# Optimization experiments

Hardware: AMD Instinct MI355X
Metric: run time of the kernel (lower is better)

Reference implementation:

```python
import jax, jax.numpy as jnp
import numpy as np

ALPHA = 0.2          # LeakyReLU negative slope
NEG = -9e15          # masking value from the torch source


def _gat_multihead(x, adj, W, a):
    """All nheads GATLayers (concat=True math, elu applied by caller).
    x: [B,N,F], adj: [B,N,N], W: [H,F,O], a: [H,2O]. Returns [B,H,N,O].
    Note a_input @ a decomposes as h_i.a[:O] + h_j.a[O:], so we never
    materialize the O(N^2 * 2O) pairwise concat tensor."""
    h = jnp.einsum('bnf,hfo->bhno', x, W)            # [B,H,N,O]
    O = h.shape[-1]
    s1 = jnp.einsum('bhno,ho->bhn', h, a[:, :O])     # h_i . a_src
    s2 = jnp.einsum('bhno,ho->bhn', h, a[:, O:])     # h_j . a_dst
    e = jax.nn.leaky_relu(s1[..., :, None] + s2[..., None, :], ALPHA)  # [B,H,N,N]
    att = jax.nn.softmax(jnp.where(adj[:, None] > 0, e, NEG), axis=-1)
    return jnp.einsum('bhij,bhjo->bhio', att, h)


def _gat_single(x, adj, W, a):
    """out_att GATLayer (concat=False, no elu). W: [F,O], a: [2O]."""
    h = jnp.einsum('bnf,fo->bno', x, W)
    O = W.shape[-1]
    s1 = h @ a[:O]
    s2 = h @ a[O:]
    e = jax.nn.leaky_relu(s1[:, :, None] + s2[:, None, :], ALPHA)
    att = jax.nn.softmax(jnp.where(adj > 0, e, NEG), axis=-1)
    return jnp.einsum('bij,bjo->bio', att, h)


def setup_inputs() -> dict:
    key = jax.random.key(0)
    ks = jax.random.split(key, 10)
    B, N, F = 2, 2048, 768
    H, O = 8, 256
    x = jax.random.normal(ks[0], (B, N, F), dtype=jnp.float32)
    # sparse-ish binary adjacency (adj>0 is all that matters) + self loops
    adj = (jax.random.uniform(ks[1], (B, N, N)) < 0.05).astype(jnp.float32)
    adj = jnp.maximum(adj, jnp.eye(N, dtype=jnp.float32)[None])
    mask = jnp.ones((B, N, 1), dtype=jnp.float32)  # unused by GAT.forward
    s = 0.05
    W_heads = jax.random.normal(ks[2], (H, F, O), dtype=jnp.float32) * s
    a_heads = jax.random.normal(ks[3], (H, 2 * O), dtype=jnp.float32) * s
    W_out = jax.random.normal(ks[4], (H * O, O), dtype=jnp.float32) * s
    a_out = jax.random.normal(ks[5], (2 * O,), dtype=jnp.float32) * s
    W_lin = jax.random.normal(ks[6], (O, H * O), dtype=jnp.float32) * s  # nn.Linear weight [out,in]
    b_lin = jnp.zeros((O,), dtype=jnp.float32)
    W_ln = jax.random.normal(ks[7], (O, O), dtype=jnp.float32) * s
    b_ln = jnp.zeros((O,), dtype=jnp.float32)
    return {"x": x, "adj": adj, "mask": mask, "W_heads": W_heads,
            "a_heads": a_heads, "W_out": W_out, "a_out": a_out,
            "W_lin": W_lin, "b_lin": b_lin, "W_ln": W_ln, "b_ln": b_ln}


def reference(x, adj, mask, W_heads, a_heads, W_out, a_out, W_lin, b_lin, W_ln, b_ln):
    # layer 0: multi-head GAT, elu, concat over heads (dropout=0 in eval)
    hp = jax.nn.elu(_gat_multihead(x, adj, W_heads, a_heads))  # [B,H,N,O]
    B, H, N, O = hp.shape
    x1 = jnp.transpose(hp, (0, 2, 1, 3)).reshape(B, N, H * O)
    # layer 1: residual linear + out_att (concat=False)
    x2 = x1 @ W_lin.T + b_lin + _gat_single(x1, adj, W_out, a_out)
    # final: relu(ln(x))
    return jax.nn.relu(x2 @ W_ln.T + b_ln)
```

## Files before the change

kernel.cpp:

```cpp
#include <hip/hip_runtime.h>
#include <hip/hip_bf16.h>

constexpr int Bb = 2, Nn = 2048, Ff = 768, Hh = 8, Oo = 256;

typedef __attribute__((ext_vector_type(8)))  short   short8;
typedef __attribute__((ext_vector_type(16))) float   f32x16;
typedef __attribute__((ext_vector_type(4)))  unsigned short ushort4_t;

__device__ inline unsigned short f2bf(float f) {
    unsigned u = __float_as_uint(f);
    u = (u + 0x7FFFu + ((u >> 16) & 1u)) >> 16;
    return (unsigned short)u;
}

__device__ inline void wfrag_kn_body(
        const float* __restrict__ W, unsigned short* __restrict__ out,
        int K, int N, int fblk, int t) {
    int f = fblk * 4 + (t >> 6);
    int slot = t & 63, kh = slot >> 5, lm = slot & 31;
    int nfk = K >> 4;
    int nt = f / nfk, kt = f - nt * nfk;
    const float* wp = W + (size_t)(kt * 16 + kh * 8) * N + nt * 32 + lm;
    ushort4_t o0, o1;
    o0.x = f2bf(wp[0]);             o0.y = f2bf(wp[(size_t)N]);
    o0.z = f2bf(wp[2 * (size_t)N]); o0.w = f2bf(wp[3 * (size_t)N]);
    o1.x = f2bf(wp[4 * (size_t)N]); o1.y = f2bf(wp[5 * (size_t)N]);
    o1.z = f2bf(wp[6 * (size_t)N]); o1.w = f2bf(wp[7 * (size_t)N]);
    unsigned short* op = out + (size_t)f * 512 + slot * 8;
    *(ushort4_t*)op = o0;
    *(ushort4_t*)(op + 4) = o1;
}

__device__ inline void wfrag_nk_body(
        const float* __restrict__ W, unsigned short* __restrict__ out,
        int K, int fblk, int t) {
    int f = fblk * 4 + (t >> 6);
    int slot = t & 63, kh = slot >> 5, lm = slot & 31;
    int nfk = K >> 4;
    int nt = f / nfk, kt = f - nt * nfk;
    const float* wp = W + (size_t)(nt * 32 + lm) * K + kt * 16 + kh * 8;
    float4 a = *(const float4*)wp, b = *(const float4*)(wp + 4);
    ushort4_t o0, o1;
    o0.x = f2bf(a.x); o0.y = f2bf(a.y); o0.z = f2bf(a.z); o0.w = f2bf(a.w);
    o1.x = f2bf(b.x); o1.y = f2bf(b.y); o1.z = f2bf(b.z); o1.w = f2bf(b.w);
    unsigned short* op = out + (size_t)f * 512 + slot * 8;
    *(ushort4_t*)op = o0;
    *(ushort4_t*)(op + 4) = o1;
}

__global__ __launch_bounds__(256) void prep_misc_kernel(
        const float* __restrict__ adj, unsigned long long* __restrict__ bits,
        const float* __restrict__ x, unsigned short* __restrict__ x_bf,
        const float* __restrict__ W_heads, unsigned short* __restrict__ WhF,
        const float* __restrict__ W_out,   unsigned short* __restrict__ WoF,
        const float* __restrict__ W_lin,   unsigned short* __restrict__ WlF,
        const float* __restrict__ W_ln,    unsigned short* __restrict__ WnF) {
    int blk = blockIdx.x, t = threadIdx.x;
    if (blk < 32768) {
        size_t gid = (size_t)blk * 256 + t;
        float v = adj[gid];
        unsigned long long m = __ballot(v > 0.f);
        if ((t & 63) == 0) bits[gid >> 6] = m;
    } else if (blk < 35840) {
        size_t i = (size_t)(blk - 32768) * 256 + t;
        float4 v = ((const float4*)x)[i];
        ushort4_t o;
        o.x = f2bf(v.x); o.y = f2bf(v.y); o.z = f2bf(v.z); o.w = f2bf(v.w);
        ((ushort4_t*)x_bf)[i] = o;
    } else if (blk < 36608) {
        int idx = blk - 35840;
        int head = idx / 96, fblk = idx - head * 96;
        wfrag_kn_body(W_heads + (size_t)head * Ff * Oo, WhF + (size_t)head * 384 * 512,
                      Ff, Oo, fblk, t);
    } else if (blk < 36864) {
        wfrag_kn_body(W_out, WoF, Hh * Oo, Oo, blk - 36608, t);
    } else if (blk < 37120) {
        wfrag_nk_body(W_lin, WlF, Hh * Oo, blk - 36864, t);
    } else {
        wfrag_nk_body(W_ln, WnF, Oo, blk - 37120, t);
    }
}

template<int SWAPZ>
__global__ __launch_bounds__(256) void gemm32_kernel(
        const unsigned short* __restrict__ A, int K, long long sA, int bAshift,
        const unsigned short* __restrict__ BF, long long sB, int bmask,
        float* __restrict__ C, long long sC,
        unsigned short* __restrict__ CF, long long sCF, int Mtot,
        const float* __restrict__ bias, int mode,
        const float* __restrict__ aall, int amask,
        float* __restrict__ E1p, float* __restrict__ E1n, float2* __restrict__ E2pn) {
    int z  = SWAPZ ? blockIdx.x : blockIdx.z;
    int mx = SWAPZ ? blockIdx.y : blockIdx.x;
    A  += (size_t)(z >> bAshift) * sA;
    BF += (size_t)(z & bmask) * sB;
    if (C) C += (size_t)z * sC;
    if (CF) CF += (size_t)z * sCF;
    int m0 = mx * 32;
    int t = threadIdx.x;
    int wv = t >> 6, lane = t & 63;
    int lm = lane & 31, kh = lane >> 5;
    int nfk = K >> 4;
    __shared__ __align__(16) unsigned short As[32][136];
    f32x16 acc[2] = {};
    int sr = t >> 3, sc2 = (t & 7) * 16;
    const unsigned short* ag  = A + (size_t)(m0 + sr) * K + sc2;
    const unsigned short* bg0 = BF + (size_t)(wv * 2) * nfk * 512;
    const unsigned short* bg1 = bg0 + (size_t)nfk * 512;
    for (int k0 = 0; k0 < K; k0 += 128) {
        *(short8*)&As[sr][sc2]     = *(const short8*)(ag + k0);
        *(short8*)&As[sr][sc2 + 8] = *(const short8*)(ag + k0 + 8);
        int kt0 = k0 >> 4;
        __syncthreads();
#pragma unroll
        for (int s = 0; s < 8; ++s) {
            short8 a0 = *(const short8*)&As[lm][s * 16 + kh * 8];
            short8 b0 = *(const short8*)(bg0 + (size_t)(kt0 + s) * 512 + lane * 8);
            short8 b1 = *(const short8*)(bg1 + (size_t)(kt0 + s) * 512 + lane * 8);
            acc[0] = __builtin_amdgcn_mfma_f32_32x32x16_bf16(a0, b0, acc[0], 0, 0, 0);
            acc[1] = __builtin_amdgcn_mfma_f32_32x32x16_bf16(a0, b1, acc[1], 0, 0, 0);
        }
        __syncthreads();
    }
#pragma unroll
    for (int nt = 0; nt < 2; ++nt) {
        int colg = wv * 64 + nt * 32 + lm;
        float bv = (mode == 2) ? bias[colg] : 0.f;
        if (C) {
#pragma unroll
            for (int reg = 0; reg < 16; ++reg) {
                int rl = 4 * kh + (reg & 3) + 8 * (reg >> 2);
                float v = acc[nt][reg];
                if (mode == 2) { v += bv; v = fmaxf(v, 0.f); }
                C[(size_t)(m0 + rl) * 256 + colg] = v;
            }
        }
        if (mode == 1) {
#pragma unroll
            for (int q = 0; q < 4; ++q) {
                int kt = m0 / 16 + (q >> 1);
                size_t fi = ((size_t)(colg >> 5) * (Mtot / 16) + kt) * 512 +
                            ((q & 1) * 32 + (colg & 31)) * 8 + kh * 4;
                ushort4_t pk;
                pk.x = f2bf(acc[nt][q * 4 + 0]);
                pk.y = f2bf(acc[nt][q * 4 + 1]);
                pk.z = f2bf(acc[nt][q * 4 + 2]);
                pk.w = f2bf(acc[nt][q * 4 + 3]);
                *(ushort4_t*)(CF + fi) = pk;
            }
        }
    }
    if (aall) {
        const float* av = aall + (size_t)(z & amask) * 512;
        float a1v0 = av[wv * 64 + lm],       a1v1 = av[wv * 64 + 32 + lm];
        float a2v0 = av[256 + wv * 64 + lm], a2v1 = av[256 + wv * 64 + 32 + lm];
        float* sbuf = (float*)As;
#pragma unroll
        for (int reg = 0; reg < 16; ++reg) {
            int rl = 4 * kh + (reg & 3) + 8 * (reg >> 2);
            float v1 = acc[0][reg] * a1v0 + acc[1][reg] * a1v1;
            float v2 = acc[0][reg] * a2v0 + acc[1][reg] * a2v1;
#pragma unroll
            for (int m = 1; m <= 16; m <<= 1) {
                v1 += __shfl_xor(v1, m, 64);
                v2 += __shfl_xor(v2, m, 64);
            }
            if (lm == 0) { sbuf[rl * 8 + wv] = v1; sbuf[rl * 8 + 4 + wv] = v2; }
        }
        __syncthreads();
        if (t < 32) {
            float s1 = sbuf[t * 8] + sbuf[t * 8 + 1] + sbuf[t * 8 + 2] + sbuf[t * 8 + 3];
            float s2 = sbuf[t * 8 + 4] + sbuf[t * 8 + 5] + sbuf[t * 8 + 6] + sbuf[t * 8 + 7];
            size_t ei = (size_t)z * Nn + m0 + t;
            E1p[ei] = __expf(s1);
            E1n[ei] = __expf(0.2f * s1);
            E2pn[ei] = make_float2(__expf(s2), __expf(0.2f * s2));
        }
    }
}

__global__ __launch_bounds__(256) void gemm32_dual_kernel(
        const unsigned short* __restrict__ A, int K, long long sA,
        const unsigned short* __restrict__ BF,
        unsigned short* __restrict__ h2f, float* __restrict__ lin,
        const float* __restrict__ a_out,
        float* __restrict__ E1p, float* __restrict__ E1n, float2* __restrict__ E2pn) {
    int b = blockIdx.z, ng = blockIdx.y;
    A += (size_t)b * sA;
    int nfk = K >> 4;
    BF += (size_t)ng * 8 * nfk * 512;
    int m0 = blockIdx.x * 32;
    int t = threadIdx.x;
    int wv = t >> 6, lane = t & 63;
    int lm = lane & 31, kh = lane >> 5;
    __shared__ __align__(16) unsigned short As[32][136];
    f32x16 acc[2] = {};
    int sr = t >> 3, sc2 = (t & 7) * 16;
    const unsigned short* ag  = A + (size_t)(m0 + sr) * K + sc2;
    const unsigned short* bg0 = BF + (size_t)(wv * 2) * nfk * 512;
    const unsigned short* bg1 = bg0 + (size_t)nfk * 512;
    for (int k0 = 0; k0 < K; k0 += 128) {
        *(short8*)&As[sr][sc2]     = *(const short8*)(ag + k0);
        *(short8*)&As[sr][sc2 + 8] = *(const short8*)(ag + k0 + 8);
        int kt0 = k0 >> 4;
        __syncthreads();
#pragma unroll
        for (int s = 0; s < 8; ++s) {
            short8 a0 = *(const short8*)&As[lm][s * 16 + kh * 8];
            short8 b0 = *(const short8*)(bg0 + (size_t)(kt0 + s) * 512 + lane * 8);
            short8 b1 = *(const short8*)(bg1 + (size_t)(kt0 + s) * 512 + lane * 8);
            acc[0] = __builtin_amdgcn_mfma_f32_32x32x16_bf16(a0, b0, acc[0], 0, 0, 0);
            acc[1] = __builtin_amdgcn_mfma_f32_32x32x16_bf16(a0, b1, acc[1], 0, 0, 0);
        }
        __syncthreads();
    }
    if (ng == 1) {
        float* C = lin + (size_t)b * Nn * 256;
#pragma unroll
        for (int nt = 0; nt < 2; ++nt) {
            int colg = wv * 64 + nt * 32 + lm;
#pragma unroll
            for (int reg = 0; reg < 16; ++reg) {
                int rl = 4 * kh + (reg & 3) + 8 * (reg >> 2);
                C[(size_t)(m0 + rl) * 256 + colg] = acc[nt][reg];
            }
        }
    } else {
        unsigned short* CF = h2f + (size_t)b * 524288;
#pragma unroll
        for (int nt = 0; nt < 2; ++nt) {
            int colg = wv * 64 + nt * 32 + lm;
#pragma unroll
            for (int q = 0; q < 4; ++q) {
                int kt = m0 / 16 + (q >> 1);
                size_t fi = ((size_t)(colg >> 5) * 128 + kt) * 512 +
                            ((q & 1) * 32 + (colg & 31)) * 8 + kh * 4;
                ushort4_t pk;
                pk.x = f2bf(acc[nt][q * 4 + 0]);
                pk.y = f2bf(acc[nt][q * 4 + 1]);
                pk.z = f2bf(acc[nt][q * 4 + 2]);
                pk.w = f2bf(acc[nt][q * 4 + 3]);
                *(ushort4_t*)(CF + fi) = pk;
            }
        }
        float a1v0 = a_out[wv * 64 + lm],       a1v1 = a_out[wv * 64 + 32 + lm];
        float a2v0 = a_out[256 + wv * 64 + lm], a2v1 = a_out[256 + wv * 64 + 32 + lm];
        float* sbuf = (float*)As;
#pragma unroll
        for (int reg = 0; reg < 16; ++reg) {
            int rl = 4 * kh + (reg & 3) + 8 * (reg >> 2);
            float v1 = acc[0][reg] * a1v0 + acc[1][reg] * a1v1;
            float v2 = acc[0][reg] * a2v0 + acc[1][reg] * a2v1;
#pragma unroll
            for (int m = 1; m <= 16; m <<= 1) {
                v1 += __shfl_xor(v1, m, 64);
                v2 += __shfl_xor(v2, m, 64);
            }
            if (lm == 0) { sbuf[rl * 8 + wv] = v1; sbuf[rl * 8 + 4 + wv] = v2; }
        }
        __syncthreads();
        if (t < 32) {
            float s1 = sbuf[t * 8] + sbuf[t * 8 + 1] + sbuf[t * 8 + 2] + sbuf[t * 8 + 3];
            float s2 = sbuf[t * 8 + 4] + sbuf[t * 8 + 5] + sbuf[t * 8 + 6] + sbuf[t * 8 + 7];
            size_t ei = (size_t)b * Nn + m0 + t;
            E1p[ei] = __expf(s1);
            E1n[ei] = __expf(0.2f * s1);
            E2pn[ei] = make_float2(__expf(s2), __expf(0.2f * s2));
        }
    }
}

__global__ __launch_bounds__(256) void gemm32_final_kernel(
        const float* __restrict__ pacc, const float* __restrict__ plsum,
        const float* __restrict__ lin, const float* __restrict__ b_lin,
        const unsigned short* __restrict__ BF, const float* __restrict__ b_ln,
        float* __restrict__ out) {
    int b = blockIdx.z;
    int m0 = blockIdx.x * 32;
    int t = threadIdx.x;
    int wv = t >> 6, lane = t & 63;
    int lm = lane & 31, kh = lane >> 5;
    constexpr int nfk = 16;
    __shared__ __align__(16) unsigned short As[32][136];
    f32x16 acc[2] = {};
    int sr = t >> 3, sc2 = (t & 7) * 16;
    int row = m0 + sr;
    int BN = Bb * Nn;
    size_t prow = (size_t)b * Nn + row;
    float li = 1.f / (plsum[prow] + plsum[prow + BN] + plsum[prow + 2 * BN] + plsum[prow + 3 * BN]);
    size_t ps4 = (size_t)Bb * Nn * 256;
    const unsigned short* bg0 = BF + (size_t)(wv * 2) * nfk * 512;
    const unsigned short* bg1 = bg0 + (size_t)nfk * 512;
    for (int k0 = 0; k0 < 256; k0 += 128) {
        int o = k0 + sc2;
        size_t pidx = prow * 256 + o;
#pragma unroll
        for (int g = 0; g < 4; ++g) {
            float4 s4 = *(const float4*)(pacc + pidx + 4 * g);
#pragma unroll
            for (int k = 1; k < 4; ++k) {
                float4 q = *(const float4*)(pacc + k * ps4 + pidx + 4 * g);
                s4.x += q.x; s4.y += q.y; s4.z += q.z; s4.w += q.w;
            }
            float4 lv = *(const float4*)(lin + pidx + 4 * g);
            float4 bv = *(const float4*)(b_lin + o + 4 * g);
            ushort4_t pk;
            pk.x = f2bf(s4.x * li + lv.x + bv.x);
            pk.y = f2bf(s4.y * li + lv.y + bv.y);
            pk.z = f2bf(s4.z * li + lv.z + bv.z);
            pk.w = f2bf(s4.w * li + lv.w + bv.w);
            *(ushort4_t*)&As[sr][sc2 + 4 * g] = pk;
        }
        int kt0 = k0 >> 4;
        __syncthreads();
#pragma unroll
        for (int s = 0; s < 8; ++s) {
            short8 a0 = *(const short8*)&As[lm][s * 16 + kh * 8];
            short8 b0 = *(const short8*)(bg0 + (size_t)(kt0 + s) * 512 + lane * 8);
            short8 b1 = *(const short8*)(bg1 + (size_t)(kt0 + s) * 512 + lane * 8);
            acc[0] = __builtin_amdgcn_mfma_f32_32x32x16_bf16(a0, b0, acc[0], 0, 0, 0);
            acc[1] = __builtin_amdgcn_mfma_f32_32x32x16_bf16(a0, b1, acc[1], 0, 0, 0);
        }
        __syncthreads();
    }
    float* C = out + (size_t)b * Nn * 256;
#pragma unroll
    for (int nt = 0; nt < 2; ++nt) {
        int colg = wv * 64 + nt * 32 + lm;
        float bv = b_ln[colg];
#pragma unroll
        for (int reg = 0; reg < 16; ++reg) {
            int rl = 4 * kh + (reg & 3) + 8 * (reg >> 2);
            float v = fmaxf(acc[nt][reg] + bv, 0.f);
            C[(size_t)(m0 + rl) * 256 + colg] = v;
        }
    }
}

template<int JLEN, int MODE, int SWAPXY>
__global__ __launch_bounds__(256, 4) void attn_v8_kernel(
        const unsigned short* __restrict__ hfrag,
        const unsigned* __restrict__ bits,
        const float* __restrict__ E1p, const float* __restrict__ E1n,
        const float2* __restrict__ E2pn,
        unsigned short* __restrict__ outbf, int ldo,
        float* __restrict__ pacc, float* __restrict__ plsum,
        int hshift) {
    constexpr int W = JLEN / 32, NC = JLEN / 64, ABS = W + 1;
    int it = SWAPXY ? blockIdx.y : blockIdx.x;
    int bh = SWAPXY ? blockIdx.x : blockIdx.y;
    int js = blockIdx.z;
    int b = bh >> hshift, hd = bh & ((1 << hshift) - 1);
    int i0 = it * 32, jbase = js * JLEN;
    int kt0 = js * (JLEN / 16);
    int t = threadIdx.x, lane = t & 63;
    int wv = t >> 6, lm = lane & 31, kh = lane >> 5;
    int ti = t & 31, jq = t >> 5;

    __shared__ unsigned ab[32 * ABS];
    __shared__ __align__(16) unsigned short ps[2][32][64];
    __shared__ float lred[32][9];
    __shared__ float linv[32];

    const unsigned* bb = bits + ((size_t)b * Nn + i0) * 64 + (jbase >> 5);
    for (int k = t; k < 32 * W; k += 256) {
        int r = k / W, w0 = k - r * W;
        ab[r * ABS + w0] = bb[(size_t)r * 64 + w0];
    }
    __syncthreads();

    float e1p = E1p[(size_t)bh * Nn + i0 + ti];
    float e1n = E1n[(size_t)bh * Nn + i0 + ti];
    const float4* e2base = (const float4*)(E2pn + (size_t)bh * Nn + jbase);

    const unsigned short* bg0 = hfrag + (size_t)bh * 524288 + (size_t)(wv * 2) * 128 * 512;
    const unsigned short* bg1 = bg0 + 128 * 512;

    f32x16 acc[2] = {};
    float lp0 = 0.f, lp1 = 0.f;
    short8 Bpp[2][2];

    auto loadBs = [&](int c, int s, int slot) {
        int kt = kt0 + c * 4 + s;
        Bpp[slot][0] = *(const short8*)(bg0 + (size_t)kt * 512 + lane * 8);
        Bpp[slot][1] = *(const short8*)(bg1 + (size_t)kt * 512 + lane * 8);
    };
    auto computeP = [&](int c, int buf) {
        int cj = c * 64;
        unsigned word = ab[ti * ABS + (cj >> 5) + (jq >> 2)];
        unsigned field = (word >> ((jq & 3) * 8)) & 0xffu;
        const float4* ep = e2base + ((cj + jq * 8) >> 1);
        unsigned pk[4];
#pragma unroll
        for (int u = 0; u < 4; ++u) {
            float4 q = ep[u];
            float p0 = fmaxf(e1p * q.x, e1n * q.y);
            p0 = ((field >> (2 * u)) & 1u) ? p0 : 0.f;
            float p1 = fmaxf(e1p * q.z, e1n * q.w);
            p1 = ((field >> (2 * u + 1)) & 1u) ? p1 : 0.f;
            if (u & 1) lp1 += p0 + p1; else lp0 += p0 + p1;
            __hip_bfloat162 hv = __float22bfloat162_rn(make_float2(p0, p1));
            pk[u] = *(unsigned*)&hv;
        }
        uint4 v; v.x = pk[0]; v.y = pk[1]; v.z = pk[2]; v.w = pk[3];
        *(uint4*)&ps[buf][ti][(jq ^ (ti & 7)) * 8] = v;
    };
    auto mfmaS = [&](int buf, int s, int slot) {
        int g = 2 * s + kh;
        short8 a0 = *(const short8*)&ps[buf][lm][(g ^ (lm & 7)) * 8];
        acc[0] = __builtin_amdgcn_mfma_f32_32x32x16_bf16(a0, Bpp[slot][0], acc[0], 0, 0, 0);
        acc[1] = __builtin_amdgcn_mfma_f32_32x32x16_bf16(a0, Bpp[slot][1], acc[1], 0, 0, 0);
    };

    computeP(0, 0);
    loadBs(0, 0, 0);
    __syncthreads();
    for (int c = 0; c < NC; ++c) {
        int cb = c & 1, nb = cb ^ 1;
        if (c + 1 < NC) computeP(c + 1, nb);
        loadBs(c, 1, 1);            mfmaS(cb, 0, 0);
        loadBs(c, 2, 0);            mfmaS(cb, 1, 1);
        loadBs(c, 3, 1);            mfmaS(cb, 2, 0);
        if (c + 1 < NC) loadBs(c + 1, 0, 0);
        mfmaS(cb, 3, 1);
        __syncthreads();
    }

    lred[ti][jq] = lp0 + lp1;
    __syncthreads();
    if (MODE == 0) {
        if (t < 32) {
            float s = 0.f;
#pragma unroll
            for (int k = 0; k < 8; ++k) s += lred[t][k];
            linv[t] = 1.f / s;
        }
        __syncthreads();
#pragma unroll
        for (int nt = 0; nt < 2; ++nt) {
            int o = wv * 64 + nt * 32 + lm;
#pragma unroll
            for (int reg = 0; reg < 16; ++reg) {
                int rl = 4 * kh + (reg & 3) + 8 * (reg >> 2);
                float v = acc[nt][reg] * linv[rl];
                v = v > 0.f ? v : expm1f(v);
                outbf[((size_t)b * Nn + i0 + rl) * ldo + (size_t)hd * Oo + o] = f2bf(v);
            }
        }
    } else {
        if (t < 32) {
            float s = 0.f;
#pragma unroll
            for (int k = 0; k < 8; ++k) s += lred[t][k];
            plsum[((size_t)js * Bb + b) * Nn + i0 + t] = s;
        }
        float* pa = pacc + (((size_t)js * Bb + b) * Nn) * 256;
#pragma unroll
        for (int nt = 0; nt < 2; ++nt) {
            int o = wv * 64 + nt * 32 + lm;
#pragma unroll
            for (int reg = 0; reg < 16; ++reg) {
                int rl = 4 * kh + (reg & 3) + 8 * (reg >> 2);
                pa[(size_t)(i0 + rl) * 256 + o] = acc[nt][reg];
            }
        }
    }
}

extern "C" void kernel_launch(void* const* d_in, const int* in_sizes, int n_in,
                              void* d_out, int out_size, void* d_ws, size_t ws_size,
                              hipStream_t stream) {
    const float* x       = (const float*)d_in[0];
    const float* adj     = (const float*)d_in[1];
    const float* W_heads = (const float*)d_in[3];
    const float* a_heads = (const float*)d_in[4];
    const float* W_out   = (const float*)d_in[5];
    const float* a_out   = (const float*)d_in[6];
    const float* W_lin   = (const float*)d_in[7];
    const float* b_lin   = (const float*)d_in[8];
    const float* W_ln    = (const float*)d_in[9];
    const float* b_ln    = (const float*)d_in[10];

    char* w = (char*)d_ws;
    float* pacc     = (float*)(w);
    float* lin      = (float*)(w + 33554432);
    float* E1p_mh   = (float*)(w + 41943040);
    float* E1n_mh   = (float*)(w + 42074112);
    float2* E2pn_mh = (float2*)(w + 42205184);
    float* E1p_sh   = (float*)(w + 42467328);
    float* E1n_sh   = (float*)(w + 42483712);
    float2* E2pn_sh = (float2*)(w + 42500096);
    unsigned long long* bits = (unsigned long long*)(w + 42532864);
    unsigned short* x_bf  = (unsigned short*)(w + 43581440);
    unsigned short* WhF   = (unsigned short*)(w + 49872896);
    unsigned short* WoF   = (unsigned short*)(w + 53018624);
    unsigned short* WlF   = (unsigned short*)(w + 54067200);
    unsigned short* WnF   = (unsigned short*)(w + 55115776);
    unsigned short* hfrag = (unsigned short*)(w + 55246848);
    unsigned short* h2frag= (unsigned short*)(w + 72024064);
    unsigned short* x1_bf = (unsigned short*)(w + 74121216);
    float* plsum = E1p_mh;

    prep_misc_kernel<<<37152, 256, 0, stream>>>(
        adj, bits, x, x_bf, W_heads, WhF, W_out, WoF, W_lin, WlF, W_ln, WnF);

    gemm32_kernel<1><<<dim3(Bb * Hh, Nn / 32, 1), 256, 0, stream>>>(
        x_bf, Ff, (long long)Nn * Ff, 3, WhF, 384LL * 512, 7,
        nullptr, 0, hfrag, 524288, Nn, nullptr, 1,
        a_heads, 7, E1p_mh, E1n_mh, E2pn_mh);
    attn_v8_kernel<2048, 0, 1><<<dim3(Bb * Hh, Nn / 32, 1), 256, 0, stream>>>(
        hfrag, (const unsigned*)bits, E1p_mh, E1n_mh, E2pn_mh,
        x1_bf, Hh * Oo, nullptr, nullptr, 3);
    gemm32_dual_kernel<<<dim3(Nn / 32, 2, Bb), 256, 0, stream>>>(
        x1_bf, Hh * Oo, (long long)Nn * Hh * Oo, WoF, h2frag, lin,
        a_out, E1p_sh, E1n_sh, E2pn_sh);
    attn_v8_kernel<512, 1, 0><<<dim3(Nn / 32, Bb, 4), 256, 0, stream>>>(
        h2frag, (const unsigned*)bits, E1p_sh, E1n_sh, E2pn_sh,
        nullptr, 0, pacc, plsum, 0);
    gemm32_final_kernel<<<dim3(Nn / 32, 1, Bb), 256, 0, stream>>>(
        pacc, plsum, lin, b_lin, WnF, b_ln, (float*)d_out);
}
```

Baseline: 262.4 us.

## Widen dual GEMM to 8 waves, split final GEMM columns, deepen attention B prefetch

The dual GEMM moves to 512 threads per block, with each wave owning one 32-column tile instead of two. The final GEMM grid gains a column-split dimension, so each block computes 128 output columns. Both changes raise parallelism and occupancy for these small kernels. The attention kernel now prefetches all four B fragments of the next chunk while issuing the current chunk's MFMAs, and raises wave priority around the MFMAs. In exchange, the final GEMM re-reads and re-reduces the pacc partial sums once per column split, and the attention kernel holds more registers.

Result: faster. 248.0 us (-5.5%).

```diff
diff --git a/kernel.cpp b/kernel.cpp
--- a/kernel.cpp
+++ b/kernel.cpp
@@ -179,7 +179,7 @@
     }
 }
 
-__global__ __launch_bounds__(256) void gemm32_dual_kernel(
+__global__ __launch_bounds__(512) void gemm32_dual_kernel(
         const unsigned short* __restrict__ A, int K, long long sA,
         const unsigned short* __restrict__ BF,
         unsigned short* __restrict__ h2f, float* __restrict__ lin,
@@ -194,74 +194,67 @@
     int wv = t >> 6, lane = t & 63;
     int lm = lane & 31, kh = lane >> 5;
     __shared__ __align__(16) unsigned short As[32][136];
-    f32x16 acc[2] = {};
-    int sr = t >> 3, sc2 = (t & 7) * 16;
-    const unsigned short* ag  = A + (size_t)(m0 + sr) * K + sc2;
-    const unsigned short* bg0 = BF + (size_t)(wv * 2) * nfk * 512;
-    const unsigned short* bg1 = bg0 + (size_t)nfk * 512;
+    f32x16 acc = {};
+    int sr = t >> 4, sc2 = (t & 15) * 8;
+    const unsigned short* ag = A + (size_t)(m0 + sr) * K + sc2;
+    const unsigned short* bg = BF + (size_t)wv * nfk * 512;
     for (int k0 = 0; k0 < K; k0 += 128) {
-        *(short8*)&As[sr][sc2]     = *(const short8*)(ag + k0);
-        *(short8*)&As[sr][sc2 + 8] = *(const short8*)(ag + k0 + 8);
+        *(short8*)&As[sr][sc2] = *(const short8*)(ag + k0);
         int kt0 = k0 >> 4;
         __syncthreads();
 #pragma unroll
         for (int s = 0; s < 8; ++s) {
             short8 a0 = *(const short8*)&As[lm][s * 16 + kh * 8];
-            short8 b0 = *(const short8*)(bg0 + (size_t)(kt0 + s) * 512 + lane * 8);
-            short8 b1 = *(const short8*)(bg1 + (size_t)(kt0 + s) * 512 + lane * 8);
-            acc[0] = __builtin_amdgcn_mfma_f32_32x32x16_bf16(a0, b0, acc[0], 0, 0, 0);
-            acc[1] = __builtin_amdgcn_mfma_f32_32x32x16_bf16(a0, b1, acc[1], 0, 0, 0);
-        }
-        __syncthreads();
-    }
+            short8 b0 = *(const short8*)(bg + (size_t)(kt0 + s) * 512 + lane * 8);
+            acc = __builtin_amdgcn_mfma_f32_32x32x16_bf16(a0, b0, acc, 0, 0, 0);
+        }
+        __syncthreads();
+    }
+    int colg = wv * 32 + lm;
     if (ng == 1) {
         float* C = lin + (size_t)b * Nn * 256;
 #pragma unroll
-        for (int nt = 0; nt < 2; ++nt) {
-            int colg = wv * 64 + nt * 32 + lm;
-#pragma unroll
-            for (int reg = 0; reg < 16; ++reg) {
-                int rl = 4 * kh + (reg & 3) + 8 * (reg >> 2);
-                C[(size_t)(m0 + rl) * 256 + colg] = acc[nt][reg];
-            }
+        for (int reg = 0; reg < 16; ++reg) {
+            int rl = 4 * kh + (reg & 3) + 8 * (reg >> 2);
+            C[(size_t)(m0 + rl) * 256 + colg] = acc[reg];
         }
     } else {
         unsigned short* CF = h2f + (size_t)b * 524288;
 #pragma unroll
-        for (int nt = 0; nt < 2; ++nt) {
-            int colg = wv * 64 + nt * 32 + lm;
-#pragma unroll
-            for (int q = 0; q < 4; ++q) {
-                int kt = m0 / 16 + (q >> 1);
-                size_t fi = ((size_t)(colg >> 5) * 128 + kt) * 512 +
-                            ((q & 1) * 32 + (colg & 31)) * 8 + kh * 4;
-                ushort4_t pk;
-                pk.x = f2bf(acc[nt][q * 4 + 0]);
-                pk.y = f2bf(acc[nt][q * 4 + 1]);
-                pk.z = f2bf(acc[nt][q * 4 + 2]);
-                pk.w = f2bf(acc[nt][q * 4 + 3]);
-                *(ushort4_t*)(CF + fi) = pk;
-            }
-        }
-        float a1v0 = a_out[wv * 64 + lm],       a1v1 = a_out[wv * 64 + 32 + lm];
-        float a2v0 = a_out[256 + wv * 64 + lm], a2v1 = a_out[256 + wv * 64 + 32 + lm];
+        for (int q = 0; q < 4; ++q) {
+            int kt = m0 / 16 + (q >> 1);
+            size_t fi = ((size_t)(colg >> 5) * 128 + kt) * 512 +
+                        ((q & 1) * 32 + (colg & 31)) * 8 + kh * 4;
+            ushort4_t pk;
+            pk.x = f2bf(acc[q * 4 + 0]);
+            pk.y = f2bf(acc[q * 4 + 1]);
+            pk.z = f2bf(acc[q * 4 + 2]);
+            pk.w = f2bf(acc[q * 4 + 3]);
+            *(ushort4_t*)(CF + fi) = pk;
+        }
+        float a1v = a_out[colg];
+        float a2v = a_out[256 + colg];
         float* sbuf = (float*)As;
 #pragma unroll
         for (int reg = 0; reg < 16; ++reg) {
             int rl = 4 * kh + (reg & 3) + 8 * (reg >> 2);
-            float v1 = acc[0][reg] * a1v0 + acc[1][reg] * a1v1;
-            float v2 = acc[0][reg] * a2v0 + acc[1][reg] * a2v1;
+            float v1 = acc[reg] * a1v;
+            float v2 = acc[reg] * a2v;
 #pragma unroll
             for (int m = 1; m <= 16; m <<= 1) {
                 v1 += __shfl_xor(v1, m, 64);
                 v2 += __shfl_xor(v2, m, 64);
             }
-            if (lm == 0) { sbuf[rl * 8 + wv] = v1; sbuf[rl * 8 + 4 + wv] = v2; }
+            if (lm == 0) { sbuf[rl * 16 + wv] = v1; sbuf[rl * 16 + 8 + wv] = v2; }
         }
         __syncthreads();
         if (t < 32) {
-            float s1 = sbuf[t * 8] + sbuf[t * 8 + 1] + sbuf[t * 8 + 2] + sbuf[t * 8 + 3];
-            float s2 = sbuf[t * 8 + 4] + sbuf[t * 8 + 5] + sbuf[t * 8 + 6] + sbuf[t * 8 + 7];
+            float s1 = 0.f, s2 = 0.f;
+#pragma unroll
+            for (int k = 0; k < 8; ++k) {
+                s1 += sbuf[t * 16 + k];
+                s2 += sbuf[t * 16 + 8 + k];
+            }
             size_t ei = (size_t)b * Nn + m0 + t;
             E1p[ei] = __expf(s1);
             E1n[ei] = __expf(0.2f * s1);
@@ -275,22 +268,21 @@
         const float* __restrict__ lin, const float* __restrict__ b_lin,
         const unsigned short* __restrict__ BF, const float* __restrict__ b_ln,
         float* __restrict__ out) {
-    int b = blockIdx.z;
+    int b = blockIdx.z, oc = blockIdx.y;
     int m0 = blockIdx.x * 32;
     int t = threadIdx.x;
     int wv = t >> 6, lane = t & 63;
     int lm = lane & 31, kh = lane >> 5;
     constexpr int nfk = 16;
     __shared__ __align__(16) unsigned short As[32][136];
-    f32x16 acc[2] = {};
+    f32x16 acc = {};
     int sr = t >> 3, sc2 = (t & 7) * 16;
     int row = m0 + sr;
     int BN = Bb * Nn;
     size_t prow = (size_t)b * Nn + row;
     float li = 1.f / (plsum[prow] + plsum[prow + BN] + plsum[prow + 2 * BN] + plsum[prow + 3 * BN]);
     size_t ps4 = (size_t)Bb * Nn * 256;
-    const unsigned short* bg0 = BF + (size_t)(wv * 2) * nfk * 512;
-    const unsigned short* bg1 = bg0 + (size_t)nfk * 512;
+    const unsigned short* bg = BF + (size_t)(oc * 4 + wv) * nfk * 512;
     for (int k0 = 0; k0 < 256; k0 += 128) {
         int o = k0 + sc2;
         size_t pidx = prow * 256 + o;
@@ -316,24 +308,19 @@
 #pragma unroll
         for (int s = 0; s < 8; ++s) {
             short8 a0 = *(const short8*)&As[lm][s * 16 + kh * 8];
-            short8 b0 = *(const short8*)(bg0 + (size_t)(kt0 + s) * 512 + lane * 8);
-            short8 b1 = *(const short8*)(bg1 + (size_t)(kt0 + s) * 512 + lane * 8);
-            acc[0] = __builtin_amdgcn_mfma_f32_32x32x16_bf16(a0, b0, acc[0], 0, 0, 0);
-            acc[1] = __builtin_amdgcn_mfma_f32_32x32x16_bf16(a0, b1, acc[1], 0, 0, 0);
+            short8 b0 = *(const short8*)(bg + (size_t)(kt0 + s) * 512 + lane * 8);
+            acc = __builtin_amdgcn_mfma_f32_32x32x16_bf16(a0, b0, acc, 0, 0, 0);
         }
         __syncthreads();
     }
     float* C = out + (size_t)b * Nn * 256;
-#pragma unroll
-    for (int nt = 0; nt < 2; ++nt) {
-        int colg = wv * 64 + nt * 32 + lm;
-        float bv = b_ln[colg];
-#pragma unroll
-        for (int reg = 0; reg < 16; ++reg) {
-            int rl = 4 * kh + (reg & 3) + 8 * (reg >> 2);
-            float v = fmaxf(acc[nt][reg] + bv, 0.f);
-            C[(size_t)(m0 + rl) * 256 + colg] = v;
-        }
+    int colg = oc * 128 + wv * 32 + lm;
+    float bv = b_ln[colg];
+#pragma unroll
+    for (int reg = 0; reg < 16; ++reg) {
+        int rl = 4 * kh + (reg & 3) + 8 * (reg >> 2);
+        float v = fmaxf(acc[reg] + bv, 0.f);
+        C[(size_t)(m0 + rl) * 256 + colg] = v;
     }
 }
 
@@ -378,7 +365,7 @@
 
     f32x16 acc[2] = {};
     float lp0 = 0.f, lp1 = 0.f;
-    short8 Bpp[2][2];
+    short8 Bpp[4][2];
 
     auto loadBs = [&](int c, int s, int slot) {
         int kt = kt0 + c * 4 + s;
@@ -408,22 +395,30 @@
     auto mfmaS = [&](int buf, int s, int slot) {
         int g = 2 * s + kh;
         short8 a0 = *(const short8*)&ps[buf][lm][(g ^ (lm & 7)) * 8];
+        __builtin_amdgcn_s_setprio(1);
         acc[0] = __builtin_amdgcn_mfma_f32_32x32x16_bf16(a0, Bpp[slot][0], acc[0], 0, 0, 0);
         acc[1] = __builtin_amdgcn_mfma_f32_32x32x16_bf16(a0, Bpp[slot][1], acc[1], 0, 0, 0);
+        __builtin_amdgcn_s_setprio(0);
     };
 
     computeP(0, 0);
-    loadBs(0, 0, 0);
+    loadBs(0, 0, 0); loadBs(0, 1, 1); loadBs(0, 2, 2); loadBs(0, 3, 3);
     __syncthreads();
-    for (int c = 0; c < NC; ++c) {
+    for (int c = 0; c + 1 < NC; ++c) {
         int cb = c & 1, nb = cb ^ 1;
-        if (c + 1 < NC) computeP(c + 1, nb);
-        loadBs(c, 1, 1);            mfmaS(cb, 0, 0);
-        loadBs(c, 2, 0);            mfmaS(cb, 1, 1);
-        loadBs(c, 3, 1);            mfmaS(cb, 2, 0);
-        if (c + 1 < NC) loadBs(c + 1, 0, 0);
-        mfmaS(cb, 3, 1);
-        __syncthreads();
+        computeP(c + 1, nb);
+        mfmaS(cb, 0, 0);  loadBs(c + 1, 0, 0);
+        mfmaS(cb, 1, 1);  loadBs(c + 1, 1, 1);
+        mfmaS(cb, 2, 2);  loadBs(c + 1, 2, 2);
+        mfmaS(cb, 3, 3);  loadBs(c + 1, 3, 3);
+        __syncthreads();
+    }
+    {
+        int cb = (NC - 1) & 1;
+        mfmaS(cb, 0, 0);
+        mfmaS(cb, 1, 1);
+        mfmaS(cb, 2, 2);
+        mfmaS(cb, 3, 3);
     }
 
     lred[ti][jq] = lp0 + lp1;
@@ -511,12 +506,12 @@
     attn_v8_kernel<2048, 0, 1><<<dim3(Bb * Hh, Nn / 32, 1), 256, 0, stream>>>(
         hfrag, (const unsigned*)bits, E1p_mh, E1n_mh, E2pn_mh,
         x1_bf, Hh * Oo, nullptr, nullptr, 3);
-    gemm32_dual_kernel<<<dim3(Nn / 32, 2, Bb), 256, 0, stream>>>(
+    gemm32_dual_kernel<<<dim3(Nn / 32, 2, Bb), 512, 0, stream>>>(
         x1_bf, Hh * Oo, (long long)Nn * Hh * Oo, WoF, h2frag, lin,
         a_out, E1p_sh, E1n_sh, E2pn_sh);
     attn_v8_kernel<512, 1, 0><<<dim3(Nn / 32, Bb, 4), 256, 0, stream>>>(
         h2frag, (const unsigned*)bits, E1p_sh, E1n_sh, E2pn_sh,
         nullptr, 0, pacc, plsum, 0);
-    gemm32_final_kernel<<<dim3(Nn / 32, 1, Bb), 256, 0, stream>>>(
+    gemm32_final_kernel<<<dim3(Nn / 32, 2, Bb), 256, 0, stream>>>(
         pacc, plsum, lin, b_lin, WnF, b_ln, (float*)d_out);
 }
```
